# Optimization experiments

Measured on AMD Instinct MI355X. Metric: run time of the kernel, lower is better.

Reference implementation:

```python
import jax, jax.numpy as jnp
import numpy as np

HEADS = 4
ATTN_DIM = 32
SCALE = ATTN_DIM ** -0.5
EPS = 1e-12  # F.normalize eps


def rmsnorm_chan(x, g):
    # x: (b, c, h, w); RMSNorm over channel dim: F.normalize(x, dim=1) * g * sqrt(c)
    c = x.shape[1]
    n = jnp.sqrt(jnp.sum(x * x, axis=1, keepdims=True))
    return x / jnp.maximum(n, EPS) * g[None, :, None, None] * jnp.sqrt(jnp.asarray(c, x.dtype))


def setup_inputs() -> dict:
    key = jax.random.key(0)
    ks = jax.random.split(key, 4)
    b, c, h, w = 16, 256, 64, 64
    hidden = HEADS * ATTN_DIM  # 128
    x = jax.random.normal(ks[0], (b, c, h, w), dtype=jnp.float32)
    norm_g = jnp.ones((c,), jnp.float32)
    w_qkv = jax.random.normal(ks[1], (3 * hidden, c), dtype=jnp.float32) * 0.02
    mem_kv = jax.random.normal(ks[2], (2, HEADS, ATTN_DIM, 4), dtype=jnp.float32)
    w_out = jax.random.normal(ks[3], (c, hidden), dtype=jnp.float32) * 0.02
    b_out = jnp.zeros((c,), jnp.float32)
    out_norm_g = jnp.ones((c,), jnp.float32)
    return {"x": x, "norm_g": norm_g, "w_qkv": w_qkv, "mem_kv": mem_kv,
            "w_out": w_out, "b_out": b_out, "out_norm_g": out_norm_g}


def reference(x, norm_g, w_qkv, mem_kv, w_out, b_out, out_norm_g):
    b, c, h, w = x.shape
    n = h * w
    xn = rmsnorm_chan(x, norm_g).reshape(b, c, n)  # pre-norm, flatten spatial
    # 1x1 conv (no bias) == channel matmul: (b, 3*hidden, n)
    qkv = jnp.einsum('oc,bcn->bon', w_qkv, xn)
    q, k, v = jnp.split(qkv, 3, axis=1)
    # (b, heads, d, n)
    q = q.reshape(b, HEADS, ATTN_DIM, n)
    k = k.reshape(b, HEADS, ATTN_DIM, n)
    v = v.reshape(b, HEADS, ATTN_DIM, n)
    # prepend memory kv (broadcast over batch): (b, heads, d, num_mem + n)
    mk = jnp.broadcast_to(mem_kv[0][None], (b, HEADS, ATTN_DIM, mem_kv.shape[-1]))
    mv = jnp.broadcast_to(mem_kv[1][None], (b, HEADS, ATTN_DIM, mem_kv.shape[-1]))
    k = jnp.concatenate([mk, k], axis=-1)
    v = jnp.concatenate([mv, v], axis=-1)
    q = jax.nn.softmax(q, axis=-2) * SCALE  # softmax over feature dim d
    k = jax.nn.softmax(k, axis=-1)          # softmax over token dim n
    context = jnp.einsum('bhdn,bhen->bhde', k, v)   # small d x e per head
    out = jnp.einsum('bhde,bhdn->bhen', context, q)  # (b, heads, e, n)
    out = out.reshape(b, HEADS * ATTN_DIM, h, w)
    # 1x1 conv with bias, then RMSNorm
    out = jnp.einsum('oc,bchw->bohw', w_out, out) + b_out[None, :, None, None]
    return rmsnorm_chan(out, out_norm_g)
```

## Files before the change

kernel.cpp:

```cpp
#include <hip/hip_runtime.h>
#include <hip/hip_bf16.h>

typedef __hip_bfloat16 bf16;
typedef __attribute__((ext_vector_type(8))) short bf16x8;
typedef __attribute__((ext_vector_type(4))) float floatx4;

#define NB 16
#define NC 256
#define NPIX 4096
#define NHID 128
#define NH 4
#define ND 32
#define NMEM 4
#define QSCALE 0.17677669529663687f

__device__ __forceinline__ void dma16(const void* g, void* l){
  __builtin_amdgcn_global_load_lds(
      (const __attribute__((address_space(1))) unsigned int*)g,
      (__attribute__((address_space(3))) unsigned int*)l, 16, 0, 0);
}

__global__ void k0_zero(float* __restrict__ p, int n){
  int i = blockIdx.x*256 + threadIdx.x;
  if (i < n) p[i] = 0.f;
}

__launch_bounds__(256)
__global__ void kW(const float* __restrict__ wqkv, const float* __restrict__ g,
                   bf16* __restrict__ wgpack){
  const int u = blockIdx.x*256 + threadIdx.x;
  const int s = u / 1536;
  const int r = u - s*1536;
  const int tile = r >> 6, l = r & 63;
  const int row = tile*16 + (l & 15);
  const int kb  = s*32 + (l >> 4)*8;
  const float* wp = wqkv + (size_t)row*NC + kb;
  floatx4 w0 = *(const floatx4*)wp;
  floatx4 w1 = *(const floatx4*)(wp + 4);
  floatx4 g0 = *(const floatx4*)(g + kb);
  floatx4 g1 = *(const floatx4*)(g + kb + 4);
  alignas(16) bf16 tmp[8];
  #pragma unroll
  for (int i = 0; i < 4; ++i){
    tmp[i]   = __float2bfloat16(w0[i]*g0[i]);
    tmp[4+i] = __float2bfloat16(w1[i]*g1[i]);
  }
  *(uint4*)(wgpack + (size_t)u*8) = *(const uint4*)tmp;
}

__launch_bounds__(256)
__global__ void kA(const float* __restrict__ x, const bf16* __restrict__ wgpack,
                   float* __restrict__ dout,
                   float* __restrict__ ctxu, float* __restrict__ zacc){
  __shared__ char smem alignas(16) [38144];
  bf16* Ab = (bf16*)smem;
  bf16 (*Xb)[40] = (bf16(*)[40])(smem + 24576);
  bf16 (*Pb)[72] = (bf16(*)[72])smem;
  bf16 (*Vb)[72] = (bf16(*)[72])(smem + 18432);
  float* ssqL = (float*)(smem + 36864);
  float* sL   = (float*)(smem + 37888);
  const int t = threadIdx.x;
  const int pb = blockIdx.x * 64, b = blockIdx.y;
  const int wv = t >> 6, lane = t & 63, m = lane & 15, q4 = lane >> 4;
  const int px_st = t & 63, cg_st = t >> 6;
  const float* xb = x + (size_t)b*NC*NPIX;
  float ssq = 0.f;
  floatx4 acc[6][4] = {};
  for (int s = 0; s < 8; ++s){
    __syncthreads();
    {
      const bf16* gt = wgpack + ((size_t)(s*24 + wv*6)*64 + lane)*8;
      char* lt = smem + wv*6144;
      #pragma unroll
      for (int tt = 0; tt < 6; ++tt)
        dma16(gt + tt*512, lt + tt*1024);
    }
    {
      const float* xp = xb + (size_t)(s*32 + cg_st*8)*NPIX + pb + px_st;
      alignas(16) bf16 tmp[8];
      #pragma unroll
      for (int j = 0; j < 8; ++j){
        float v = xp[(size_t)j*NPIX];
        ssq += v*v;
        tmp[j] = __float2bfloat16(v);
      }
      *(uint4*)&Xb[px_st][cg_st*8] = *(const uint4*)tmp;
    }
    __syncthreads();
    bf16x8 bfr[4];
    #pragma unroll
    for (int pt = 0; pt < 4; ++pt)
      bfr[pt] = *(const bf16x8*)&Xb[pt*16 + m][q4*8];
    #pragma unroll
    for (int rt = 0; rt < 6; ++rt){
      bf16x8 af = *(const bf16x8*)(Ab + (size_t)wv*3072 + rt*512 + (q4*16 + m)*8);
      #pragma unroll
      for (int pt = 0; pt < 4; ++pt)
        acc[rt][pt] = __builtin_amdgcn_mfma_f32_16x16x32_bf16(af, bfr[pt], acc[rt][pt], 0, 0, 0);
    }
  }
  ssqL[cg_st*64 + px_st] = ssq;
  __syncthreads();
  if (t < 64){
    float tot = ssqL[t] + ssqL[64 + t] + ssqL[128 + t] + ssqL[192 + t];
    sL[t] = 16.0f / fmaxf(sqrtf(tot), 1e-12f);
  }
  __syncthreads();
  float sv[4];
  #pragma unroll
  for (int pt = 0; pt < 4; ++pt) sv[pt] = sL[pt*16 + m];
  #pragma unroll
  for (int pr = 0; pr < 3; ++pr){
    const int ra = 2*pr, rb = 2*pr + 1;
    const int row0 = wv*96 + pr*32;
    const int type = row0 >> 7;
    if (type == 0){
      const int slice = row0 >> 5;
      const int j0 = (q4 & 1)*4;
      #pragma unroll
      for (int pt = 0; pt < 4; ++pt){
        float va[4], vb[4];
        float mx = -1e30f;
        #pragma unroll
        for (int r = 0; r < 4; ++r){
          va[r] = acc[ra][pt][r]*sv[pt];
          vb[r] = acc[rb][pt][r]*sv[pt];
          mx = fmaxf(mx, fmaxf(va[r], vb[r]));
        }
        mx = fmaxf(mx, __shfl_xor(mx, 16, 64));
        mx = fmaxf(mx, __shfl_xor(mx, 32, 64));
        float se = 0.f;
        #pragma unroll
        for (int r = 0; r < 4; ++r){
          va[r] = __expf(va[r] - mx); vb[r] = __expf(vb[r] - mx);
          se += va[r] + vb[r];
        }
        se += __shfl_xor(se, 16, 64);
        se += __shfl_xor(se, 32, 64);
        const float inv = QSCALE / se;
        alignas(8) bf16 pka[4], pkb[4];
        #pragma unroll
        for (int r = 0; r < 4; ++r){
          pka[r] = __float2bfloat16(va[r]*inv);
          pkb[r] = __float2bfloat16(vb[r]*inv);
        }
        const int ca = (slice*4 + pt)*4 + (q4 >> 1);
        const int cb = ca + 2;
        bf16* pa = (bf16*)(dout + (size_t)(b*NC + ca)*NPIX + pb) + m*8 + j0;
        bf16* pv = (bf16*)(dout + (size_t)(b*NC + cb)*NPIX + pb) + m*8 + j0;
        *(uint2*)pa = *(const uint2*)pka;
        *(uint2*)pv = *(const uint2*)pkb;
      }
    } else if (type == 1){
      const int d0 = row0 - 128;
      float za[4] = {}, zb[4] = {};
      #pragma unroll
      for (int pt = 0; pt < 4; ++pt){
        #pragma unroll
        for (int r = 0; r < 4; ++r){
          float pa = __expf(acc[ra][pt][r]*sv[pt]);
          float pv = __expf(acc[rb][pt][r]*sv[pt]);
          za[r] += pa; zb[r] += pv;
          Pb[d0      + q4*4 + r][pt*16 + m] = __float2bfloat16(pa);
          Pb[d0 + 16 + q4*4 + r][pt*16 + m] = __float2bfloat16(pv);
        }
      }
      #pragma unroll
      for (int r = 0; r < 4; ++r){
        #pragma unroll
        for (int o = 1; o < 16; o <<= 1){
          za[r] += __shfl_xor(za[r], o, 64);
          zb[r] += __shfl_xor(zb[r], o, 64);
        }
      }
      if (m == 0){
        #pragma unroll
        for (int r = 0; r < 4; ++r){
          atomicAdd(&zacc[b*NHID + d0      + q4*4 + r], za[r]);
          atomicAdd(&zacc[b*NHID + d0 + 16 + q4*4 + r], zb[r]);
        }
      }
    } else {
      const int v0 = row0 - 256;
      #pragma unroll
      for (int pt = 0; pt < 4; ++pt)
        #pragma unroll
        for (int r = 0; r < 4; ++r){
          Vb[v0      + q4*4 + r][pt*16 + m] = __float2bfloat16(acc[ra][pt][r]*sv[pt]);
          Vb[v0 + 16 + q4*4 + r][pt*16 + m] = __float2bfloat16(acc[rb][pt][r]*sv[pt]);
        }
    }
  }
  __syncthreads();
  floatx4 cx[2][2] = {};
  #pragma unroll
  for (int k0t = 0; k0t < 64; k0t += 32){
    bf16x8 af[2], bf[2];
    #pragma unroll
    for (int dt = 0; dt < 2; ++dt) af[dt] = *(const bf16x8*)&Pb[wv*32 + dt*16 + m][k0t + q4*8];
    #pragma unroll
    for (int et = 0; et < 2; ++et) bf[et] = *(const bf16x8*)&Vb[wv*32 + et*16 + m][k0t + q4*8];
    #pragma unroll
    for (int dt = 0; dt < 2; ++dt)
      #pragma unroll
      for (int et = 0; et < 2; ++et)
        cx[dt][et] = __builtin_amdgcn_mfma_f32_16x16x32_bf16(af[dt], bf[et], cx[dt][et], 0, 0, 0);
  }
  float* cb2 = ctxu + (size_t)(b*NH + wv)*ND*ND;
  #pragma unroll
  for (int dt = 0; dt < 2; ++dt)
    #pragma unroll
    for (int et = 0; et < 2; ++et)
      #pragma unroll
      for (int r = 0; r < 4; ++r)
        atomicAdd(&cb2[(dt*16 + q4*4 + r)*ND + et*16 + m], cx[dt][et][r]);
}

__launch_bounds__(256)
__global__ void k4_weff(const float* __restrict__ ctxu, const float* __restrict__ zacc,
                        const float* __restrict__ memkv, const float* __restrict__ wout,
                        bf16* __restrict__ wpack){
  const int idx = blockIdx.x*256 + threadIdx.x;
  const int b   = idx >> 15;
  const int o   = (idx >> 7) & 255;
  const int hd  = idx & 127;
  const int h = hd >> 5, d = hd & 31;
  const float* mk = memkv + hd*NMEM;
  float me[4];
  float z = zacc[b*NHID + hd];
  #pragma unroll
  for (int j = 0; j < 4; ++j){ me[j] = __expf(mk[j]); z += me[j]; }
  const float invz = 1.0f / z;
  const float* cp = ctxu + (size_t)((b*NH + h)*ND + d)*ND;
  const float* wp = wout + (size_t)o*NHID + h*ND;
  const float* mv = memkv + (size_t)(NHID + h*ND)*NMEM;
  float acc = 0.f;
  #pragma unroll
  for (int e = 0; e < ND; ++e){
    float ce = cp[e];
    #pragma unroll
    for (int j = 0; j < 4; ++j) ce += me[j]*mv[e*NMEM + j];
    acc += ce*wp[e];
  }
  const int slice = hd >> 5, q4k = (hd >> 3) & 3, j = hd & 7;
  const int tile = o >> 4, m16 = o & 15;
  wpack[((size_t)((b*4 + slice)*16 + tile)*64 + q4k*16 + m16)*8 + j] = __float2bfloat16(acc*invz);
}

__launch_bounds__(256)
__global__ void k5_out(float* dout, const bf16* __restrict__ wpack,
                       const float* __restrict__ bout, const float* __restrict__ gout){
  __shared__ char smem alignas(16) [21760];
  bf16* Wb = (bf16*)smem;
  bf16* Qb = (bf16*)(smem + 16384);
  float* red = (float*)(smem + 20480);
  float* nf  = (float*)(smem + 21504);
  const int t = threadIdx.x;
  const int pb = blockIdx.x * 64, b = blockIdx.y;
  const int wv = t >> 6, lane = t & 63, m = lane & 15, q4 = lane >> 4;
  floatx4 acc[4][4] = {};
  for (int s = 0; s < 4; ++s){
    __syncthreads();
    {
      const bf16* gt = wpack + ((size_t)((b*4 + s)*16 + wv*4)*64 + lane)*8;
      char* lt = smem + wv*4096;
      #pragma unroll
      for (int tt = 0; tt < 4; ++tt)
        dma16(gt + tt*512, lt + tt*1024);
    }
    {
      const char* gq = (const char*)(dout + (size_t)(b*NC + (s*4 + wv)*4 + q4)*NPIX + pb) + m*16;
      dma16(gq, smem + 16384 + wv*1024);
    }
    __syncthreads();
    bf16x8 bfr[4];
    #pragma unroll
    for (int pt = 0; pt < 4; ++pt)
      bfr[pt] = *(const bf16x8*)(Qb + pt*512 + (q4*16 + m)*8);
    #pragma unroll
    for (int rt = 0; rt < 4; ++rt){
      bf16x8 af = *(const bf16x8*)(Wb + (size_t)(wv*4 + rt)*512 + (q4*16 + m)*8);
      #pragma unroll
      for (int pt = 0; pt < 4; ++pt)
        acc[rt][pt] = __builtin_amdgcn_mfma_f32_16x16x32_bf16(af, bfr[pt], acc[rt][pt], 0, 0, 0);
    }
  }
  float ps[4] = {0.f, 0.f, 0.f, 0.f};
  #pragma unroll
  for (int rt = 0; rt < 4; ++rt){
    const int row = wv*64 + rt*16 + q4*4;
    #pragma unroll
    for (int r = 0; r < 4; ++r){
      const float bias = bout[row + r];
      #pragma unroll
      for (int pt = 0; pt < 4; ++pt){
        acc[rt][pt][r] += bias;
        ps[pt] += acc[rt][pt][r]*acc[rt][pt][r];
      }
    }
  }
  #pragma unroll
  for (int pt = 0; pt < 4; ++pt){
    ps[pt] += __shfl_xor(ps[pt], 16, 64);
    ps[pt] += __shfl_xor(ps[pt], 32, 64);
  }
  __syncthreads();
  if (q4 == 0){
    #pragma unroll
    for (int pt = 0; pt < 4; ++pt) red[wv*64 + pt*16 + m] = ps[pt];
  }
  __syncthreads();
  if (t < 64){
    float tot = red[t] + red[64 + t] + red[128 + t] + red[192 + t];
    nf[t] = 16.0f / fmaxf(sqrtf(tot), 1e-12f);
  }
  __syncthreads();
  float nv[4];
  #pragma unroll
  for (int pt = 0; pt < 4; ++pt) nv[pt] = nf[pt*16 + m];
  #pragma unroll
  for (int rt = 0; rt < 4; ++rt){
    const int row = wv*64 + rt*16 + q4*4;
    #pragma unroll
    for (int r = 0; r < 4; ++r){
      const float gg = gout[row + r];
      float* op = dout + (size_t)(b*NC + row + r)*NPIX + pb + m;
      #pragma unroll
      for (int pt = 0; pt < 4; ++pt)
        op[pt*16] = acc[rt][pt][r]*nv[pt]*gg;
    }
  }
}

extern "C" void kernel_launch(void* const* d_in, const int* in_sizes, int n_in,
                              void* d_out, int out_size, void* d_ws, size_t ws_size,
                              hipStream_t stream) {
  (void)in_sizes; (void)n_in; (void)out_size; (void)ws_size;
  const float* x     = (const float*)d_in[0];
  const float* ng    = (const float*)d_in[1];
  const float* wqkv  = (const float*)d_in[2];
  const float* memkv = (const float*)d_in[3];
  const float* wout  = (const float*)d_in[4];
  const float* bout  = (const float*)d_in[5];
  const float* gout  = (const float*)d_in[6];
  float* dout = (float*)d_out;
  char* ws = (char*)d_ws;
  bf16*  wgpack = (bf16*)(ws);
  bf16*  wpack  = (bf16*)(ws + 196608);
  float* ctxu   = (float*)(ws + 1245184);
  float* zacc   = (float*)(ws + 1507328);

  k0_zero<<<dim3(264),     256, 0, stream>>>(ctxu, 65536 + 2048);
  kW     <<<dim3(48),      256, 0, stream>>>(wqkv, ng, wgpack);
  kA     <<<dim3(64, 16),  256, 0, stream>>>(x, wgpack, dout, ctxu, zacc);
  k4_weff<<<dim3(2048),    256, 0, stream>>>(ctxu, zacc, memkv, wout, wpack);
  k5_out <<<dim3(64, 16),  256, 0, stream>>>(dout, wpack, bout, gout);
}
```

Baseline: 191.7 us.

## Load full x tile upfront, double-buffer weight DMA, widen kA to 512 threads

kA now runs with 512 threads. It loads all 256 channels of the 64-pixel x tile into LDS in one pass, so the RMS scale is computed before the GEMM. Weight slices are then prefetched for the next step while the current MFMAs run. The two pixel halves each build a partial context, which is reduced through LDS before the atomics, halving atomic traffic. k5_out loads its whole Q tile up front and prefetches weights one step ahead; both kernels use more LDS, which may lower occupancy.

```diff
diff --git a/kernel.cpp b/kernel.cpp
--- a/kernel.cpp
+++ b/kernel.cpp
@@ -48,35 +48,35 @@
   *(uint4*)(wgpack + (size_t)u*8) = *(const uint4*)tmp;
 }
 
-__launch_bounds__(256)
+__launch_bounds__(512, 4)
 __global__ void kA(const float* __restrict__ x, const bf16* __restrict__ wgpack,
                    float* __restrict__ dout,
                    float* __restrict__ ctxu, float* __restrict__ zacc){
-  __shared__ char smem alignas(16) [38144];
+  __shared__ char smem alignas(16) [60672];
   bf16* Ab = (bf16*)smem;
-  bf16 (*Xb)[40] = (bf16(*)[40])(smem + 24576);
+  bf16 (*Xb)[264] = (bf16(*)[264])(smem + 24576);
   bf16 (*Pb)[72] = (bf16(*)[72])smem;
   bf16 (*Vb)[72] = (bf16(*)[72])(smem + 18432);
-  float* ssqL = (float*)(smem + 36864);
-  float* sL   = (float*)(smem + 37888);
+  float* ssqL = (float*)(smem + 58368);
+  float* sL   = (float*)(smem + 60416);
+  float* cxL  = (float*)smem;
   const int t = threadIdx.x;
   const int pb = blockIdx.x * 64, b = blockIdx.y;
   const int wv = t >> 6, lane = t & 63, m = lane & 15, q4 = lane >> 4;
-  const int px_st = t & 63, cg_st = t >> 6;
+  const int rg = wv & 3, ph = wv >> 2;
   const float* xb = x + (size_t)b*NC*NPIX;
-  float ssq = 0.f;
-  floatx4 acc[6][4] = {};
-  for (int s = 0; s < 8; ++s){
-    __syncthreads();
-    {
-      const bf16* gt = wgpack + ((size_t)(s*24 + wv*6)*64 + lane)*8;
-      char* lt = smem + wv*6144;
-      #pragma unroll
-      for (int tt = 0; tt < 6; ++tt)
-        dma16(gt + tt*512, lt + tt*1024);
-    }
-    {
-      const float* xp = xb + (size_t)(s*32 + cg_st*8)*NPIX + pb + px_st;
+
+  {
+    const bf16* gt = wgpack + ((size_t)(wv*3)*64 + lane)*8;
+    char* lt = smem + wv*3072;
+    #pragma unroll
+    for (int tt = 0; tt < 3; ++tt) dma16(gt + tt*512, lt + tt*1024);
+  }
+  {
+    float ssq = 0.f;
+    #pragma unroll
+    for (int s4 = 0; s4 < 4; ++s4){
+      const float* xp = xb + (size_t)(s4*64 + wv*8)*NPIX + pb + lane;
       alignas(16) bf16 tmp[8];
       #pragma unroll
       for (int j = 0; j < 8; ++j){
@@ -84,56 +84,69 @@
         ssq += v*v;
         tmp[j] = __float2bfloat16(v);
       }
-      *(uint4*)&Xb[px_st][cg_st*8] = *(const uint4*)tmp;
-    }
+      *(uint4*)&Xb[lane][s4*64 + wv*8] = *(const uint4*)tmp;
+    }
+    ssqL[wv*64 + lane] = ssq;
+  }
+  __syncthreads();
+  if (t < 64){
+    float tot = 0.f;
+    #pragma unroll
+    for (int i = 0; i < 8; ++i) tot += ssqL[i*64 + t];
+    sL[t] = 16.0f / fmaxf(sqrtf(tot), 1e-12f);
+  }
+  floatx4 acc[6][2] = {};
+  for (int s = 0; s < 8; ++s){
+    bf16x8 bfr[2], af[6];
+    #pragma unroll
+    for (int pt = 0; pt < 2; ++pt)
+      bfr[pt] = *(const bf16x8*)&Xb[(ph*2 + pt)*16 + m][s*32 + q4*8];
+    #pragma unroll
+    for (int rt = 0; rt < 6; ++rt)
+      af[rt] = *(const bf16x8*)(Ab + (size_t)(rg*6 + rt)*512 + (q4*16 + m)*8);
     __syncthreads();
-    bf16x8 bfr[4];
-    #pragma unroll
-    for (int pt = 0; pt < 4; ++pt)
-      bfr[pt] = *(const bf16x8*)&Xb[pt*16 + m][q4*8];
-    #pragma unroll
-    for (int rt = 0; rt < 6; ++rt){
-      bf16x8 af = *(const bf16x8*)(Ab + (size_t)wv*3072 + rt*512 + (q4*16 + m)*8);
-      #pragma unroll
-      for (int pt = 0; pt < 4; ++pt)
-        acc[rt][pt] = __builtin_amdgcn_mfma_f32_16x16x32_bf16(af, bfr[pt], acc[rt][pt], 0, 0, 0);
-    }
-  }
-  ssqL[cg_st*64 + px_st] = ssq;
-  __syncthreads();
-  if (t < 64){
-    float tot = ssqL[t] + ssqL[64 + t] + ssqL[128 + t] + ssqL[192 + t];
-    sL[t] = 16.0f / fmaxf(sqrtf(tot), 1e-12f);
-  }
-  __syncthreads();
-  float sv[4];
-  #pragma unroll
-  for (int pt = 0; pt < 4; ++pt) sv[pt] = sL[pt*16 + m];
+    if (s < 7){
+      const bf16* gt = wgpack + ((size_t)((s+1)*24 + wv*3)*64 + lane)*8;
+      char* lt = smem + wv*3072;
+      #pragma unroll
+      for (int tt = 0; tt < 3; ++tt) dma16(gt + tt*512, lt + tt*1024);
+    }
+    #pragma unroll
+    for (int rt = 0; rt < 6; ++rt)
+      #pragma unroll
+      for (int pt = 0; pt < 2; ++pt)
+        acc[rt][pt] = __builtin_amdgcn_mfma_f32_16x16x32_bf16(af[rt], bfr[pt], acc[rt][pt], 0, 0, 0);
+    __syncthreads();
+  }
+  float sv[2];
+  #pragma unroll
+  for (int pt = 0; pt < 2; ++pt) sv[pt] = sL[(ph*2 + pt)*16 + m];
   #pragma unroll
   for (int pr = 0; pr < 3; ++pr){
     const int ra = 2*pr, rb = 2*pr + 1;
-    const int row0 = wv*96 + pr*32;
+    const int row0 = rg*96 + pr*32;
     const int type = row0 >> 7;
     if (type == 0){
       const int slice = row0 >> 5;
       const int j0 = (q4 & 1)*4;
       #pragma unroll
-      for (int pt = 0; pt < 4; ++pt){
-        float va[4], vb[4];
+      for (int pt = 0; pt < 2; ++pt){
+        const int gpt = ph*2 + pt;
+        float va[4], vb4[4];
         float mx = -1e30f;
         #pragma unroll
         for (int r = 0; r < 4; ++r){
-          va[r] = acc[ra][pt][r]*sv[pt];
-          vb[r] = acc[rb][pt][r]*sv[pt];
-          mx = fmaxf(mx, fmaxf(va[r], vb[r]));
+          va[r]  = acc[ra][pt][r]*sv[pt];
+          vb4[r] = acc[rb][pt][r]*sv[pt];
+          mx = fmaxf(mx, fmaxf(va[r], vb4[r]));
         }
         mx = fmaxf(mx, __shfl_xor(mx, 16, 64));
         mx = fmaxf(mx, __shfl_xor(mx, 32, 64));
         float se = 0.f;
         #pragma unroll
         for (int r = 0; r < 4; ++r){
-          va[r] = __expf(va[r] - mx); vb[r] = __expf(vb[r] - mx);
-          se += va[r] + vb[r];
+          va[r] = __expf(va[r] - mx); vb4[r] = __expf(vb4[r] - mx);
+          se += va[r] + vb4[r];
         }
         se += __shfl_xor(se, 16, 64);
         se += __shfl_xor(se, 32, 64);
@@ -142,9 +155,9 @@
         #pragma unroll
         for (int r = 0; r < 4; ++r){
           pka[r] = __float2bfloat16(va[r]*inv);
-          pkb[r] = __float2bfloat16(vb[r]*inv);
-        }
-        const int ca = (slice*4 + pt)*4 + (q4 >> 1);
+          pkb[r] = __float2bfloat16(vb4[r]*inv);
+        }
+        const int ca = (slice*4 + gpt)*4 + (q4 >> 1);
         const int cb = ca + 2;
         bf16* pa = (bf16*)(dout + (size_t)(b*NC + ca)*NPIX + pb) + m*8 + j0;
         bf16* pv = (bf16*)(dout + (size_t)(b*NC + cb)*NPIX + pb) + m*8 + j0;
@@ -155,14 +168,15 @@
       const int d0 = row0 - 128;
       float za[4] = {}, zb[4] = {};
       #pragma unroll
-      for (int pt = 0; pt < 4; ++pt){
+      for (int pt = 0; pt < 2; ++pt){
+        const int gpt = ph*2 + pt;
         #pragma unroll
         for (int r = 0; r < 4; ++r){
           float pa = __expf(acc[ra][pt][r]*sv[pt]);
           float pv = __expf(acc[rb][pt][r]*sv[pt]);
           za[r] += pa; zb[r] += pv;
-          Pb[d0      + q4*4 + r][pt*16 + m] = __float2bfloat16(pa);
-          Pb[d0 + 16 + q4*4 + r][pt*16 + m] = __float2bfloat16(pv);
+          Pb[d0      + q4*4 + r][gpt*16 + m] = __float2bfloat16(pa);
+          Pb[d0 + 16 + q4*4 + r][gpt*16 + m] = __float2bfloat16(pv);
         }
       }
       #pragma unroll
@@ -183,37 +197,53 @@
     } else {
       const int v0 = row0 - 256;
       #pragma unroll
-      for (int pt = 0; pt < 4; ++pt)
-        #pragma unroll
-        for (int r = 0; r < 4; ++r){
-          Vb[v0      + q4*4 + r][pt*16 + m] = __float2bfloat16(acc[ra][pt][r]*sv[pt]);
-          Vb[v0 + 16 + q4*4 + r][pt*16 + m] = __float2bfloat16(acc[rb][pt][r]*sv[pt]);
-        }
+      for (int pt = 0; pt < 2; ++pt){
+        const int gpt = ph*2 + pt;
+        #pragma unroll
+        for (int r = 0; r < 4; ++r){
+          Vb[v0      + q4*4 + r][gpt*16 + m] = __float2bfloat16(acc[ra][pt][r]*sv[pt]);
+          Vb[v0 + 16 + q4*4 + r][gpt*16 + m] = __float2bfloat16(acc[rb][pt][r]*sv[pt]);
+        }
+      }
     }
   }
   __syncthreads();
   floatx4 cx[2][2] = {};
-  #pragma unroll
-  for (int k0t = 0; k0t < 64; k0t += 32){
-    bf16x8 af[2], bf[2];
-    #pragma unroll
-    for (int dt = 0; dt < 2; ++dt) af[dt] = *(const bf16x8*)&Pb[wv*32 + dt*16 + m][k0t + q4*8];
-    #pragma unroll
-    for (int et = 0; et < 2; ++et) bf[et] = *(const bf16x8*)&Vb[wv*32 + et*16 + m][k0t + q4*8];
+  {
+    const int k0t = ph*32;
+    bf16x8 paf[2], pvf[2];
+    #pragma unroll
+    for (int dt = 0; dt < 2; ++dt) paf[dt] = *(const bf16x8*)&Pb[rg*32 + dt*16 + m][k0t + q4*8];
+    #pragma unroll
+    for (int et = 0; et < 2; ++et) pvf[et] = *(const bf16x8*)&Vb[rg*32 + et*16 + m][k0t + q4*8];
     #pragma unroll
     for (int dt = 0; dt < 2; ++dt)
       #pragma unroll
       for (int et = 0; et < 2; ++et)
-        cx[dt][et] = __builtin_amdgcn_mfma_f32_16x16x32_bf16(af[dt], bf[et], cx[dt][et], 0, 0, 0);
-  }
-  float* cb2 = ctxu + (size_t)(b*NH + wv)*ND*ND;
-  #pragma unroll
-  for (int dt = 0; dt < 2; ++dt)
-    #pragma unroll
-    for (int et = 0; et < 2; ++et)
-      #pragma unroll
-      for (int r = 0; r < 4; ++r)
-        atomicAdd(&cb2[(dt*16 + q4*4 + r)*ND + et*16 + m], cx[dt][et][r]);
+        cx[dt][et] = __builtin_amdgcn_mfma_f32_16x16x32_bf16(paf[dt], pvf[et], cx[dt][et], 0, 0, 0);
+  }
+  __syncthreads();
+  if (ph == 1){
+    #pragma unroll
+    for (int dt = 0; dt < 2; ++dt)
+      #pragma unroll
+      for (int et = 0; et < 2; ++et)
+        #pragma unroll
+        for (int r = 0; r < 4; ++r)
+          cxL[rg*1024 + (dt*16 + q4*4 + r)*32 + et*16 + m] = cx[dt][et][r];
+  }
+  __syncthreads();
+  if (ph == 0){
+    float* cb2 = ctxu + (size_t)(b*NH + rg)*ND*ND;
+    #pragma unroll
+    for (int dt = 0; dt < 2; ++dt)
+      #pragma unroll
+      for (int et = 0; et < 2; ++et)
+        #pragma unroll
+        for (int r = 0; r < 4; ++r)
+          atomicAdd(&cb2[(dt*16 + q4*4 + r)*ND + et*16 + m],
+                    cx[dt][et][r] + cxL[rg*1024 + (dt*16 + q4*4 + r)*32 + et*16 + m]);
+  }
 }
 
 __launch_bounds__(256)
@@ -247,43 +277,54 @@
   wpack[((size_t)((b*4 + slice)*16 + tile)*64 + q4k*16 + m16)*8 + j] = __float2bfloat16(acc*invz);
 }
 
-__launch_bounds__(256)
+__launch_bounds__(256, 4)
 __global__ void k5_out(float* dout, const bf16* __restrict__ wpack,
                        const float* __restrict__ bout, const float* __restrict__ gout){
-  __shared__ char smem alignas(16) [21760];
+  __shared__ char smem alignas(16) [34048];
   bf16* Wb = (bf16*)smem;
   bf16* Qb = (bf16*)(smem + 16384);
-  float* red = (float*)(smem + 20480);
-  float* nf  = (float*)(smem + 21504);
+  float* red = (float*)(smem + 32768);
+  float* nf  = (float*)(smem + 33792);
   const int t = threadIdx.x;
   const int pb = blockIdx.x * 64, b = blockIdx.y;
   const int wv = t >> 6, lane = t & 63, m = lane & 15, q4 = lane >> 4;
+  {
+    #pragma unroll
+    for (int i = 0; i < 4; ++i){
+      const int tau = wv*4 + i;
+      const char* gq = (const char*)(dout + (size_t)(b*NC + tau*4 + q4)*NPIX + pb) + m*16;
+      dma16(gq, smem + 16384 + tau*1024);
+    }
+  }
+  {
+    const bf16* gt = wpack + ((size_t)((b*4)*16 + wv*4)*64 + lane)*8;
+    char* lt = smem + wv*4096;
+    #pragma unroll
+    for (int tt = 0; tt < 4; ++tt) dma16(gt + tt*512, lt + tt*1024);
+  }
+  __syncthreads();
   floatx4 acc[4][4] = {};
   for (int s = 0; s < 4; ++s){
+    bf16x8 bfr[4], af[4];
+    #pragma unroll
+    for (int pt = 0; pt < 4; ++pt)
+      bfr[pt] = *(const bf16x8*)(Qb + (size_t)(s*4 + pt)*512 + (q4*16 + m)*8);
+    #pragma unroll
+    for (int rt = 0; rt < 4; ++rt)
+      af[rt] = *(const bf16x8*)(Wb + (size_t)(wv*4 + rt)*512 + (q4*16 + m)*8);
     __syncthreads();
-    {
-      const bf16* gt = wpack + ((size_t)((b*4 + s)*16 + wv*4)*64 + lane)*8;
+    if (s < 3){
+      const bf16* gt = wpack + ((size_t)((b*4 + s+1)*16 + wv*4)*64 + lane)*8;
       char* lt = smem + wv*4096;
       #pragma unroll
-      for (int tt = 0; tt < 4; ++tt)
-        dma16(gt + tt*512, lt + tt*1024);
-    }
-    {
-      const char* gq = (const char*)(dout + (size_t)(b*NC + (s*4 + wv)*4 + q4)*NPIX + pb) + m*16;
-      dma16(gq, smem + 16384 + wv*1024);
-    }
+      for (int tt = 0; tt < 4; ++tt) dma16(gt + tt*512, lt + tt*1024);
+    }
+    #pragma unroll
+    for (int rt = 0; rt < 4; ++rt)
+      #pragma unroll
+      for (int pt = 0; pt < 4; ++pt)
+        acc[rt][pt] = __builtin_amdgcn_mfma_f32_16x16x32_bf16(af[rt], bfr[pt], acc[rt][pt], 0, 0, 0);
     __syncthreads();
-    bf16x8 bfr[4];
-    #pragma unroll
-    for (int pt = 0; pt < 4; ++pt)
-      bfr[pt] = *(const bf16x8*)(Qb + pt*512 + (q4*16 + m)*8);
-    #pragma unroll
-    for (int rt = 0; rt < 4; ++rt){
-      bf16x8 af = *(const bf16x8*)(Wb + (size_t)(wv*4 + rt)*512 + (q4*16 + m)*8);
-      #pragma unroll
-      for (int pt = 0; pt < 4; ++pt)
-        acc[rt][pt] = __builtin_amdgcn_mfma_f32_16x16x32_bf16(af, bfr[pt], acc[rt][pt], 0, 0, 0);
-    }
   }
   float ps[4] = {0.f, 0.f, 0.f, 0.f};
   #pragma unroll
@@ -352,7 +393,7 @@
 
   k0_zero<<<dim3(264),     256, 0, stream>>>(ctxu, 65536 + 2048);
   kW     <<<dim3(48),      256, 0, stream>>>(wqkv, ng, wgpack);
-  kA     <<<dim3(64, 16),  256, 0, stream>>>(x, wgpack, dout, ctxu, zacc);
+  kA     <<<dim3(64, 16),  512, 0, stream>>>(x, wgpack, dout, ctxu, zacc);
   k4_weff<<<dim3(2048),    256, 0, stream>>>(ctxu, zacc, memkv, wout, wpack);
   k5_out <<<dim3(64, 16),  256, 0, stream>>>(dout, wpack, bout, gout);
 }
```

Result: slower. 203.2 us (+6.0%).

## Double-buffer LDS staging in QKV projection and output projection kernels

Applied to the files above, without the earlier changes.

The QKV projection kernel now stages the weight tiles and the converted x tiles into two LDS buffers, prefetching step s+1 while MFMAs run on step s, with one barrier per iteration instead of two. The output kernel loads the whole Q/activation tile once up front and double-buffers the per-slice weight tiles the same way. The goal is to overlap global-to-LDS transfer latency with matrix compute. The cost is much more shared memory per block (about 60 KB and 50 KB), which can lower occupancy. The synchronous x loads inside the prefetch may still stall before the MFMAs are issued.

```diff
diff --git a/kernel.cpp b/kernel.cpp
--- a/kernel.cpp
+++ b/kernel.cpp
@@ -52,41 +52,44 @@
 __global__ void kA(const float* __restrict__ x, const bf16* __restrict__ wgpack,
                    float* __restrict__ dout,
                    float* __restrict__ ctxu, float* __restrict__ zacc){
-  __shared__ char smem alignas(16) [38144];
-  bf16* Ab = (bf16*)smem;
-  bf16 (*Xb)[40] = (bf16(*)[40])(smem + 24576);
+  __shared__ char smem alignas(16) [60672];
   bf16 (*Pb)[72] = (bf16(*)[72])smem;
   bf16 (*Vb)[72] = (bf16(*)[72])(smem + 18432);
-  float* ssqL = (float*)(smem + 36864);
-  float* sL   = (float*)(smem + 37888);
+  float* ssqL = (float*)(smem + 59392);
+  float* sL   = (float*)(smem + 60416);
   const int t = threadIdx.x;
   const int pb = blockIdx.x * 64, b = blockIdx.y;
   const int wv = t >> 6, lane = t & 63, m = lane & 15, q4 = lane >> 4;
   const int px_st = t & 63, cg_st = t >> 6;
   const float* xb = x + (size_t)b*NC*NPIX;
   float ssq = 0.f;
+
+  auto stage = [&](int s, int buf){
+    const bf16* gt = wgpack + ((size_t)(s*24 + wv*6)*64 + lane)*8;
+    char* lt = smem + buf*24576 + wv*6144;
+    #pragma unroll
+    for (int tt = 0; tt < 6; ++tt)
+      dma16(gt + tt*512, lt + tt*1024);
+    const float* xp = xb + (size_t)(s*32 + cg_st*8)*NPIX + pb + px_st;
+    alignas(16) bf16 tmp[8];
+    #pragma unroll
+    for (int j = 0; j < 8; ++j){
+      float v = xp[(size_t)j*NPIX];
+      ssq += v*v;
+      tmp[j] = __float2bfloat16(v);
+    }
+    bf16 (*Xb)[40] = (bf16(*)[40])(smem + 49152 + buf*5120);
+    *(uint4*)&Xb[px_st][cg_st*8] = *(const uint4*)tmp;
+  };
+
+  stage(0, 0);
+  __syncthreads();
   floatx4 acc[6][4] = {};
   for (int s = 0; s < 8; ++s){
-    __syncthreads();
-    {
-      const bf16* gt = wgpack + ((size_t)(s*24 + wv*6)*64 + lane)*8;
-      char* lt = smem + wv*6144;
-      #pragma unroll
-      for (int tt = 0; tt < 6; ++tt)
-        dma16(gt + tt*512, lt + tt*1024);
-    }
-    {
-      const float* xp = xb + (size_t)(s*32 + cg_st*8)*NPIX + pb + px_st;
-      alignas(16) bf16 tmp[8];
-      #pragma unroll
-      for (int j = 0; j < 8; ++j){
-        float v = xp[(size_t)j*NPIX];
-        ssq += v*v;
-        tmp[j] = __float2bfloat16(v);
-      }
-      *(uint4*)&Xb[px_st][cg_st*8] = *(const uint4*)tmp;
-    }
-    __syncthreads();
+    const int buf = s & 1;
+    if (s < 7) stage(s + 1, buf ^ 1);
+    bf16 (*Xb)[40] = (bf16(*)[40])(smem + 49152 + buf*5120);
+    const bf16* Ab = (const bf16*)(smem + buf*24576);
     bf16x8 bfr[4];
     #pragma unroll
     for (int pt = 0; pt < 4; ++pt)
@@ -98,6 +101,7 @@
       for (int pt = 0; pt < 4; ++pt)
         acc[rt][pt] = __builtin_amdgcn_mfma_f32_16x16x32_bf16(af, bfr[pt], acc[rt][pt], 0, 0, 0);
     }
+    __syncthreads();
   }
   ssqL[cg_st*64 + px_st] = ssq;
   __syncthreads();
@@ -250,40 +254,51 @@
 __launch_bounds__(256)
 __global__ void k5_out(float* dout, const bf16* __restrict__ wpack,
                        const float* __restrict__ bout, const float* __restrict__ gout){
-  __shared__ char smem alignas(16) [21760];
-  bf16* Wb = (bf16*)smem;
-  bf16* Qb = (bf16*)(smem + 16384);
-  float* red = (float*)(smem + 20480);
-  float* nf  = (float*)(smem + 21504);
+  __shared__ char smem alignas(16) [50432];
+  bf16* Qb = (bf16*)(smem + 32768);
+  float* red = (float*)(smem + 49152);
+  float* nf  = (float*)(smem + 50176);
   const int t = threadIdx.x;
   const int pb = blockIdx.x * 64, b = blockIdx.y;
   const int wv = t >> 6, lane = t & 63, m = lane & 15, q4 = lane >> 4;
+  {
+    #pragma unroll
+    for (int i = 0; i < 4; ++i){
+      const int tau = wv*4 + i;
+      const char* gq = (const char*)(dout + (size_t)(b*NC + tau*4 + q4)*NPIX + pb) + m*16;
+      dma16(gq, smem + 32768 + tau*1024);
+    }
+  }
+  {
+    const bf16* gt = wpack + ((size_t)((b*4)*16 + wv*4)*64 + lane)*8;
+    char* lt = smem + wv*4096;
+    #pragma unroll
+    for (int tt = 0; tt < 4; ++tt) dma16(gt + tt*512, lt + tt*1024);
+  }
+  __syncthreads();
   floatx4 acc[4][4] = {};
   for (int s = 0; s < 4; ++s){
+    const int buf = s & 1;
+    if (s < 3){
+      const bf16* gt = wpack + ((size_t)((b*4 + s+1)*16 + wv*4)*64 + lane)*8;
+      char* lt = smem + (buf^1)*16384 + wv*4096;
+      #pragma unroll
+      for (int tt = 0; tt < 4; ++tt) dma16(gt + tt*512, lt + tt*1024);
+    }
+    const bf16* Wb = (const bf16*)(smem + buf*16384);
+    bf16x8 bfr[4], af[4];
+    #pragma unroll
+    for (int pt = 0; pt < 4; ++pt)
+      bfr[pt] = *(const bf16x8*)(Qb + (size_t)(s*4 + pt)*512 + (q4*16 + m)*8);
+    #pragma unroll
+    for (int rt = 0; rt < 4; ++rt)
+      af[rt] = *(const bf16x8*)(Wb + (size_t)(wv*4 + rt)*512 + (q4*16 + m)*8);
+    #pragma unroll
+    for (int rt = 0; rt < 4; ++rt)
+      #pragma unroll
+      for (int pt = 0; pt < 4; ++pt)
+        acc[rt][pt] = __builtin_amdgcn_mfma_f32_16x16x32_bf16(af[rt], bfr[pt], acc[rt][pt], 0, 0, 0);
     __syncthreads();
-    {
-      const bf16* gt = wpack + ((size_t)((b*4 + s)*16 + wv*4)*64 + lane)*8;
-      char* lt = smem + wv*4096;
-      #pragma unroll
-      for (int tt = 0; tt < 4; ++tt)
-        dma16(gt + tt*512, lt + tt*1024);
-    }
-    {
-      const char* gq = (const char*)(dout + (size_t)(b*NC + (s*4 + wv)*4 + q4)*NPIX + pb) + m*16;
-      dma16(gq, smem + 16384 + wv*1024);
-    }
-    __syncthreads();
-    bf16x8 bfr[4];
-    #pragma unroll
-    for (int pt = 0; pt < 4; ++pt)
-      bfr[pt] = *(const bf16x8*)(Qb + pt*512 + (q4*16 + m)*8);
-    #pragma unroll
-    for (int rt = 0; rt < 4; ++rt){
-      bf16x8 af = *(const bf16x8*)(Wb + (size_t)(wv*4 + rt)*512 + (q4*16 + m)*8);
-      #pragma unroll
-      for (int pt = 0; pt < 4; ++pt)
-        acc[rt][pt] = __builtin_amdgcn_mfma_f32_16x16x32_bf16(af, bfr[pt], acc[rt][pt], 0, 0, 0);
-    }
   }
   float ps[4] = {0.f, 0.f, 0.f, 0.f};
   #pragma unroll
@@ -304,7 +319,6 @@
     ps[pt] += __shfl_xor(ps[pt], 16, 64);
     ps[pt] += __shfl_xor(ps[pt], 32, 64);
   }
-  __syncthreads();
   if (q4 == 0){
     #pragma unroll
     for (int pt = 0; pt < 4; ++pt) red[wv*64 + pt*16 + m] = ps[pt];
```

After: 188.3 us. Within noise of the previous version (-1.8%).
